# Kernel optimization log

Measured on AMD Instinct MI355X. Metric: run time of the kernel, lower is better.

Reference implementation:

```python
import jax, jax.numpy as jnp
import numpy as np

D_HEAD = 64
KV_HEADS = 8
Q_HEADS = 32
ROPE_BASE = 10000.0


def rope(x):
    # x: (B, S, H, D); pairs are interleaved along last dim, matching torch view(...,D//2,2)
    B, S, H, D = x.shape
    inv_freq = 1.0 / (ROPE_BASE ** (jnp.arange(0, D, 2, dtype=jnp.float32) / D))
    theta = jnp.arange(S, dtype=jnp.float32)[:, None] * inv_freq[None, :]  # (S, D/2)
    cos = jnp.cos(theta)[None, :, None, :]
    sin = jnp.sin(theta)[None, :, None, :]
    xf = x.astype(jnp.float32).reshape(B, S, H, D // 2, 2)
    x1, x2 = xf[..., 0], xf[..., 1]
    out = jnp.stack((x1 * cos - x2 * sin, x1 * sin + x2 * cos), axis=-1)
    return out.reshape(B, S, H, D).astype(x.dtype)


def setup_inputs() -> dict:
    key = jax.random.key(0)
    ks = jax.random.split(key, 5)
    B, S, D = 2, 2048, 2048
    scale = 1.0 / np.sqrt(D)
    return {
        "x": jax.random.normal(ks[0], (B, S, D), dtype=jnp.float32),
        "Wq": jax.random.normal(ks[1], (Q_HEADS * D_HEAD, D), dtype=jnp.float32) * scale,
        "Wk": jax.random.normal(ks[2], (KV_HEADS * D_HEAD, D), dtype=jnp.float32) * scale,
        "Wv": jax.random.normal(ks[3], (KV_HEADS * D_HEAD, D), dtype=jnp.float32) * scale,
        "Wo": jax.random.normal(ks[4], (D, D), dtype=jnp.float32) * scale,
    }


def reference(x, Wq, Wk, Wv, Wo):
    B, S, D = x.shape
    G = Q_HEADS // KV_HEADS  # query heads per kv head

    Q = (x @ Wq.T).reshape(B, S, Q_HEADS, D_HEAD)
    K = (x @ Wk.T).reshape(B, S, KV_HEADS, D_HEAD)
    V = (x @ Wv.T).reshape(B, S, KV_HEADS, D_HEAD)

    Q = rope(Q)
    K = rope(K)

    # (B, KV, G, S, Dh): group g of kv head h corresponds to q head h*G+g,
    # exactly matching repeat_interleave of K/V along head dim.
    Q = Q.transpose(0, 2, 1, 3).reshape(B, KV_HEADS, G, S, D_HEAD)
    K = K.transpose(0, 2, 1, 3)  # (B, KV, S, Dh)
    V = V.transpose(0, 2, 1, 3)

    scores = jnp.einsum("bkgsd,bktd->bkgst", Q, K) / np.sqrt(D_HEAD).astype(np.float32)
    causal_mask = jnp.tril(jnp.ones((S, S), dtype=bool))
    scores = jnp.where(causal_mask, scores, -jnp.inf)
    probs = jax.nn.softmax(scores, axis=-1)
    attn = jnp.einsum("bkgst,bktd->bkgsd", probs, V)

    attn = attn.reshape(B, Q_HEADS, S, D_HEAD).transpose(0, 2, 1, 3).reshape(B, S, D)
    return attn @ Wo.T
```

## Files before the change

### kernel.cpp

```cpp
#include <hip/hip_runtime.h>
#include <stdint.h>

#define S_LEN   2048
#define D_MODEL 2048
#define DKV     512

typedef __attribute__((ext_vector_type(8))) short short8;
typedef __attribute__((ext_vector_type(4))) float f32x4;
typedef __attribute__((ext_vector_type(4))) unsigned uint4v;

__device__ static inline unsigned short f2bf(float f) {
  unsigned u = __builtin_bit_cast(unsigned, f);
  u += 0x7FFFu + ((u >> 16) & 1u);
  return (unsigned short)(u >> 16);
}
__device__ static inline float bf2f(unsigned short h) {
  return __builtin_bit_cast(float, ((unsigned)h) << 16);
}
__device__ static inline unsigned packtrunc2(float f0, float f1) {
  return __builtin_amdgcn_perm(__builtin_bit_cast(unsigned, f1),
                               __builtin_bit_cast(unsigned, f0), 0x07060302u);
}

__device__ static inline void gload_lds16(const void* g, void* lds) {
  __builtin_amdgcn_global_load_lds((const __attribute__((address_space(1))) void*)g,
                                   (__attribute__((address_space(3))) void*)lds,
                                   16, 0, 0);
}

template <int N>
__device__ __forceinline__ void wait_vm() {
  if constexpr (N == 8)      asm volatile("s_waitcnt vmcnt(8)" ::: "memory");
  else if constexpr (N == 6) asm volatile("s_waitcnt vmcnt(6)" ::: "memory");
  else if constexpr (N == 4) asm volatile("s_waitcnt vmcnt(4)" ::: "memory");
  else if constexpr (N == 3) asm volatile("s_waitcnt vmcnt(3)" ::: "memory");
  else                       asm volatile("s_waitcnt vmcnt(0)" ::: "memory");
}

__device__ static inline void pl32swap(unsigned& a, unsigned& b) {
  asm volatile("v_permlane32_swap_b32 %0, %1" : "+v"(a), "+v"(b));
}
__device__ static inline void pl16swap(unsigned& a, unsigned& b) {
  asm volatile("v_permlane16_swap_b32 %0, %1" : "+v"(a), "+v"(b));
}

__global__ __launch_bounds__(256) void cvt_all_kernel(
    const float* __restrict__ x, const float* __restrict__ wq, const float* __restrict__ wk,
    const float* __restrict__ wv, const float* __restrict__ wo,
    unsigned short* __restrict__ xb, unsigned short* __restrict__ wqb,
    unsigned short* __restrict__ wkb, unsigned short* __restrict__ wvb,
    unsigned short* __restrict__ wob) {
  int i = blockIdx.x * 256 + threadIdx.x;
  const float* s; unsigned short* d;
  if (i < 1048576)      { s = x;  d = xb;  }
  else if (i < 1572864) { s = wq; d = wqb; i -= 1048576; }
  else if (i < 1703936) { s = wk; d = wkb; i -= 1572864; }
  else if (i < 1835008) { s = wv; d = wvb; i -= 1703936; }
  else                  { s = wo; d = wob; i -= 1835008; }
  const float4 a = ((const float4*)s)[i * 2];
  const float4 b = ((const float4*)s)[i * 2 + 1];
  unsigned short u[8] = {f2bf(a.x), f2bf(a.y), f2bf(a.z), f2bf(a.w),
                         f2bf(b.x), f2bf(b.y), f2bf(b.z), f2bf(b.w)};
  *(uint4*)(d + (size_t)i * 8) = *(const uint4*)u;
}

template <int BM, int CMODE, typename CT>
__device__ __forceinline__ void gemm_deep_body(
    const unsigned short* __restrict__ A, int lda,
    const unsigned short* __restrict__ B, int ldb,
    CT* __restrict__ C, int ldc, int m0, int n0, unsigned short* ldsu) {
  constexpr int MI = BM / 32;
  constexpr int NI = 4;
  constexpr int A_BYTES = BM * 64;
  constexpr int B_BYTES = 256 * 64;
  constexpr int TILE_BYTES = A_BYTES + B_BYTES;
  constexpr int AL = BM / 128;
  constexpr int LOADS = AL + 2;
  constexpr int VMS = 2 * LOADS;

  const int tid  = threadIdx.x;
  const int lane = tid & 63;
  const int w    = tid >> 6;
  const int wm   = w >> 2;
  const int wn   = w & 3;
  const int lcol = lane & 15;
  const int lq   = lane >> 4;
  char* const ldsb = (char*)ldsu;

  const int sl   = (lane & 7) ^ (lane >> 3);
  const int colg = (sl & 3) * 8;
  const unsigned short* gA[AL];
  const unsigned short* gB[2];
#pragma unroll
  for (int L = 0; L < AL; ++L) {
    const int r = 2 * (L * 64 + w * 8 + (lane >> 3)) + (sl >> 2);
    gA[L] = A + (size_t)(m0 + r) * lda + colg;
  }
#pragma unroll
  for (int L = 0; L < 2; ++L) {
    const int r = 2 * (L * 64 + w * 8 + (lane >> 3)) + (sl >> 2);
    gB[L] = B + (size_t)(n0 + r) * ldb + colg;
  }

  auto stage = [&](int tt) {
    char* const sb = ldsb + (tt & 3) * TILE_BYTES;
#pragma unroll
    for (int L = 0; L < AL; ++L)
      gload_lds16(gA[L] + tt * 32, sb + L * 8192 + w * 1024);
#pragma unroll
    for (int L = 0; L < 2; ++L)
      gload_lds16(gB[L] + tt * 32, sb + A_BYTES + L * 8192 + w * 1024);
  };

  const int sR    = (((lcol & 1) << 2) | lq) ^ ((lcol >> 1) & 7);
  const int rdoff = (lcol >> 1) * 128 + sR * 16;

  f32x4 acc[MI][NI] = {};

  auto compute_tile = [&](char* buf) {
    short8 af[MI], bfr[NI];
#pragma unroll
    for (int mi = 0; mi < MI; ++mi)
      af[mi] = *(const short8*)(buf + wm * (MI * 1024) + mi * 1024 + rdoff);
#pragma unroll
    for (int ni = 0; ni < NI; ++ni)
      bfr[ni] = *(const short8*)(buf + A_BYTES + wn * 4096 + ni * 1024 + rdoff);
    __builtin_amdgcn_s_setprio(1);
#pragma unroll
    for (int mi = 0; mi < MI; ++mi)
#pragma unroll
      for (int ni = 0; ni < NI; ++ni)
        acc[mi][ni] = __builtin_amdgcn_mfma_f32_16x16x32_bf16(af[mi], bfr[ni], acc[mi][ni], 0, 0, 0);
    __builtin_amdgcn_s_setprio(0);
  };

  stage(0); stage(1); stage(2);

#define GPHASE(T, VMW, DOSTG)                          \
  do {                                                 \
    wait_vm<VMW>();                                    \
    __builtin_amdgcn_s_barrier();                      \
    asm volatile("" ::: "memory");                     \
    __builtin_amdgcn_sched_barrier(0);                 \
    if (DOSTG) stage((T) + 3);                         \
    compute_tile(ldsb + ((T) & 3) * TILE_BYTES);       \
  } while (0)

  for (int t4 = 0; t4 < 15; ++t4) {
    const int t = t4 * 4;
    GPHASE(t + 0, VMS, true);
    GPHASE(t + 1, VMS, true);
    GPHASE(t + 2, VMS, true);
    GPHASE(t + 3, VMS, true);
  }
  GPHASE(60, VMS,   true);
  GPHASE(61, VMS,   false);
  GPHASE(62, LOADS, false);
  GPHASE(63, 0,     false);
#undef GPHASE

#pragma unroll
  for (int mi = 0; mi < MI; ++mi)
#pragma unroll
    for (int ni = 0; ni < NI; ++ni)
#pragma unroll
      for (int r = 0; r < 4; ++r) {
        const int row = m0 + wm * (MI * 16) + mi * 16 + lq * 4 + r;
        const int col = n0 + wn * 64 + ni * 16 + lcol;
        if constexpr (CMODE == 1) {
          C[((size_t)((row >> 11) * 512 + col)) * 2048 + (row & 2047)] = f2bf(acc[mi][ni][r]);
        } else if constexpr (CMODE == 2) {
          C[(size_t)row * ldc + col] = acc[mi][ni][r];
        } else {
          C[(size_t)row * ldc + col] = f2bf(acc[mi][ni][r]);
        }
      }
}

__global__ __launch_bounds__(512, 2) void qkv_gemm_kernel(
    const unsigned short* __restrict__ x,
    const unsigned short* __restrict__ Wq, const unsigned short* __restrict__ Wk,
    const unsigned short* __restrict__ Wv,
    unsigned short* __restrict__ Qo, unsigned short* __restrict__ Ko,
    unsigned short* __restrict__ Vt) {
  extern __shared__ __align__(16) unsigned short lds[];
  const int bid = blockIdx.x;
  const int swz = (bid & 7) * 24 + (bid >> 3);
  const int mt = swz / 12, nt = swz % 12;
  const int m0 = mt * 256;
  if (nt < 8)
    gemm_deep_body<256, 0, unsigned short>(x, D_MODEL, Wq, D_MODEL, Qo, D_MODEL, m0, nt * 256, lds);
  else if (nt < 10)
    gemm_deep_body<256, 0, unsigned short>(x, D_MODEL, Wk, D_MODEL, Ko, DKV, m0, (nt - 8) * 256, lds);
  else
    gemm_deep_body<256, 1, unsigned short>(x, D_MODEL, Wv, D_MODEL, Vt, DKV, m0, (nt - 10) * 256, lds);
}

__global__ __launch_bounds__(512, 2) void oproj_gemm_kernel(
    const unsigned short* __restrict__ A, const unsigned short* __restrict__ Wo,
    float* __restrict__ C) {
  extern __shared__ __align__(16) unsigned short lds[];
  const int bid = blockIdx.x;
  const int swz = (bid & 7) * 32 + (bid >> 3);
  const int mt = swz >> 3, nt = swz & 7;
  gemm_deep_body<128, 2, float>(A, D_MODEL, Wo, D_MODEL, C, D_MODEL, mt * 128, nt * 256, lds);
}

__global__ __launch_bounds__(256) void rope_both_kernel(unsigned short* __restrict__ Qb,
                                                        unsigned short* __restrict__ Kb) {
  int idx = blockIdx.x * 256 + threadIdx.x;
  unsigned short* X; int lgHalf; float scale;
  if (idx < 4194304) { X = Qb; lgHalf = 10; scale = 0.1803368801111244f; }
  else               { X = Kb; lgHalf = 8;  scale = 1.0f; idx -= 4194304; }
  const int half = 1 << lgHalf;
  const int r  = idx >> lgHalf;
  const int cp = idx & (half - 1);
  const int i  = cp & 31;
  const int s  = r & (S_LEN - 1);
  const float inv = exp2f(-13.287712379549449f * (float)(2 * i) * (1.0f / 64.0f));
  const float th  = (float)s * inv;
  const float c = cosf(th), sn = sinf(th);
  unsigned short* p = X + ((size_t)r << (lgHalf + 1)) + 2 * cp;
  const float x0 = bf2f(p[0]), x1 = bf2f(p[1]);
  p[0] = f2bf((x0 * c - x1 * sn) * scale);
  p[1] = f2bf((x0 * sn + x1 * c) * scale);
}

#define SOFTMAX_FRAG(Sv, lac, pf)                                              \
  do {                                                                         \
    float e0 = __builtin_amdgcn_exp2f(Sv[0][0]);                               \
    float e1 = __builtin_amdgcn_exp2f(Sv[0][1]);                               \
    float e2 = __builtin_amdgcn_exp2f(Sv[0][2]);                               \
    float e3 = __builtin_amdgcn_exp2f(Sv[0][3]);                               \
    unsigned dd0 = packtrunc2(e0, e1), dd1 = packtrunc2(e2, e3);               \
    lac += (e0 + e1) + (e2 + e3);                                              \
    e0 = __builtin_amdgcn_exp2f(Sv[1][0]);                                     \
    e1 = __builtin_amdgcn_exp2f(Sv[1][1]);                                     \
    e2 = __builtin_amdgcn_exp2f(Sv[1][2]);                                     \
    e3 = __builtin_amdgcn_exp2f(Sv[1][3]);                                     \
    unsigned dd2 = packtrunc2(e0, e1), dd3 = packtrunc2(e2, e3);               \
    lac += (e0 + e1) + (e2 + e3);                                              \
    e0 = __builtin_amdgcn_exp2f(Sv[2][0]);                                     \
    e1 = __builtin_amdgcn_exp2f(Sv[2][1]);                                     \
    e2 = __builtin_amdgcn_exp2f(Sv[2][2]);                                     \
    e3 = __builtin_amdgcn_exp2f(Sv[2][3]);                                     \
    unsigned dd4 = packtrunc2(e0, e1), dd5 = packtrunc2(e2, e3);               \
    lac += (e0 + e1) + (e2 + e3);                                              \
    e0 = __builtin_amdgcn_exp2f(Sv[3][0]);                                     \
    e1 = __builtin_amdgcn_exp2f(Sv[3][1]);                                     \
    e2 = __builtin_amdgcn_exp2f(Sv[3][2]);                                     \
    e3 = __builtin_amdgcn_exp2f(Sv[3][3]);                                     \
    unsigned dd6 = packtrunc2(e0, e1), dd7 = packtrunc2(e2, e3);               \
    lac += (e0 + e1) + (e2 + e3);                                              \
    pl32swap(dd0, dd2); pl32swap(dd1, dd3);                                    \
    pl32swap(dd4, dd6); pl32swap(dd5, dd7);                                    \
    pl16swap(dd0, dd2); pl16swap(dd1, dd3);                                    \
    pl16swap(dd4, dd6); pl16swap(dd5, dd7);                                    \
    const uint4v va_ = {dd0, dd1, dd2, dd3};                                   \
    const uint4v vb_ = {dd4, dd5, dd6, dd7};                                   \
    pf##0 = __builtin_bit_cast(short8, va_);                                   \
    pf##1 = __builtin_bit_cast(short8, vb_);                                   \
  } while (0)

__global__ __launch_bounds__(256, 2) void attn_kernel(const unsigned short* __restrict__ Q,
                                                      const unsigned short* __restrict__ K,
                                                      const unsigned short* __restrict__ Vt,
                                                      unsigned short* __restrict__ O) {
  const int hq = blockIdx.y;
  const int bb = blockIdx.z;
  const int hk = hq >> 2;
  const int tid  = threadIdx.x;
  const int lane = tid & 63;
  const int w    = tid >> 6;
  const int lcol = lane & 15;
  const int lq   = lane >> 4;
  const int trow = tid >> 2;
  const int tq   = (tid & 3) * 16;

  const int X   = blockIdx.x;
  const int qt0 = X, qt1 = 31 - X;

  __shared__ unsigned short Ks[2][64 * 72];
  __shared__ unsigned short Vts[2][64 * 72];

  const int prow = w * 16 + lcol;

  short8 qf00, qf01, qf10, qf11;
  {
    const unsigned short* g0 = Q + ((size_t)(bb * S_LEN + qt0 * 64 + prow)) * D_MODEL + hq * 64;
    const unsigned short* g1 = Q + ((size_t)(bb * S_LEN + qt1 * 64 + prow)) * D_MODEL + hq * 64;
    qf00 = *(const short8*)(g0 + lq * 8);
    qf01 = *(const short8*)(g0 + 32 + lq * 8);
    qf10 = *(const short8*)(g1 + lq * 8);
    qf11 = *(const short8*)(g1 + 32 + lq * 8);
  }

  uint4 kp0, kp1, vp0, vp1;
  {
    const unsigned short* gk = K + ((size_t)(bb * S_LEN + trow)) * DKV + hk * 64 + tq;
    kp0 = *(const uint4*)gk; kp1 = *(const uint4*)(gk + 8);
    const unsigned short* gv = Vt + ((size_t)(bb * DKV + hk * 64 + trow)) * S_LEN + tq;
    vp0 = *(const uint4*)gv; vp1 = *(const uint4*)(gv + 8);
  }

  f32x4 Oacc[2][4] = {};
  float lacc0 = 0.f, lacc1 = 0.f;

  const int tmax = qt1;
  for (int t = 0; t <= tmax; ++t) {
    const int bs = t & 1;
    *(uint4*)&Ks[bs][trow * 72 + tq]      = kp0;
    *(uint4*)&Ks[bs][trow * 72 + tq + 8]  = kp1;
    *(uint4*)&Vts[bs][trow * 72 + tq]     = vp0;
    *(uint4*)&Vts[bs][trow * 72 + tq + 8] = vp1;
    if (t < tmax) {
      const int t1 = (t + 1) * 64;
      const unsigned short* gk = K + ((size_t)(bb * S_LEN + t1 + trow)) * DKV + hk * 64 + tq;
      kp0 = *(const uint4*)gk; kp1 = *(const uint4*)(gk + 8);
      const unsigned short* gv = Vt + ((size_t)(bb * DKV + hk * 64 + trow)) * S_LEN + t1 + tq;
      vp0 = *(const uint4*)gv; vp1 = *(const uint4*)(gv + 8);
    }
    asm volatile("s_waitcnt lgkmcnt(0)" ::: "memory");
    __builtin_amdgcn_s_barrier();
    __builtin_amdgcn_sched_barrier(0);

    const bool a0 = (t <= qt0);

    f32x4 S0[4] = {}, S1[4] = {};
#pragma unroll
    for (int ks = 0; ks < 2; ++ks)
#pragma unroll
      for (int nt = 0; nt < 4; ++nt) {
        const short8 kf = *(const short8*)&Ks[bs][(nt * 16 + lcol) * 72 + ks * 32 + lq * 8];
        const short8 q0 = ks ? qf01 : qf00;
        const short8 q1 = ks ? qf11 : qf10;
        if (a0) S0[nt] = __builtin_amdgcn_mfma_f32_16x16x32_bf16(kf, q0, S0[nt], 0, 0, 0);
        S1[nt] = __builtin_amdgcn_mfma_f32_16x16x32_bf16(kf, q1, S1[nt], 0, 0, 0);
      }

    if (t == qt0) {
#pragma unroll
      for (int nt = 0; nt < 4; ++nt)
#pragma unroll
        for (int r = 0; r < 4; ++r)
          if (nt * 16 + lq * 4 + r > prow) S0[nt][r] = -1e30f;
    }
    if (t == qt1) {
#pragma unroll
      for (int nt = 0; nt < 4; ++nt)
#pragma unroll
        for (int r = 0; r < 4; ++r)
          if (nt * 16 + lq * 4 + r > prow) S1[nt][r] = -1e30f;
    }

    short8 pf00, pf01, pf10, pf11;
    if (a0) SOFTMAX_FRAG(S0, lacc0, pf0);
    SOFTMAX_FRAG(S1, lacc1, pf1);

#pragma unroll
    for (int ks = 0; ks < 2; ++ks)
#pragma unroll
      for (int dt = 0; dt < 4; ++dt) {
        const short8 vf = *(const short8*)&Vts[bs][(dt * 16 + lcol) * 72 + ks * 32 + lq * 8];
        const short8 p0 = ks ? pf01 : pf00;
        const short8 p1 = ks ? pf11 : pf10;
        if (a0) Oacc[0][dt] = __builtin_amdgcn_mfma_f32_16x16x32_bf16(vf, p0, Oacc[0][dt], 0, 0, 0);
        Oacc[1][dt] = __builtin_amdgcn_mfma_f32_16x16x32_bf16(vf, p1, Oacc[1][dt], 0, 0, 0);
      }
  }

  const int qts[2] = {qt0, qt1};
  const float laccs[2] = {lacc0, lacc1};
#pragma unroll
  for (int j = 0; j < 2; ++j) {
    float l = laccs[j];
    l += __shfl_xor(l, 16);
    l += __shfl_xor(l, 32);
    const float inv = 1.0f / l;
    const int qrow = qts[j] * 64 + prow;
#pragma unroll
    for (int dt = 0; dt < 4; ++dt) {
      unsigned short u[4] = {f2bf(Oacc[j][dt][0] * inv), f2bf(Oacc[j][dt][1] * inv),
                             f2bf(Oacc[j][dt][2] * inv), f2bf(Oacc[j][dt][3] * inv)};
      *(uint2*)&O[(size_t)(bb * S_LEN + qrow) * D_MODEL + hq * 64 + dt * 16 + lq * 4] =
          *(const uint2*)u;
    }
  }
}

extern "C" void kernel_launch(void* const* d_in, const int* in_sizes, int n_in,
                              void* d_out, int out_size, void* d_ws, size_t ws_size,
                              hipStream_t stream) {
  const float* x  = (const float*)d_in[0];
  const float* Wq = (const float*)d_in[1];
  const float* Wk = (const float*)d_in[2];
  const float* Wv = (const float*)d_in[3];
  const float* Wo = (const float*)d_in[4];
  float* out = (float*)d_out;

  unsigned short* Qb  = (unsigned short*)d_ws;
  unsigned short* Kb  = Qb  + (size_t)4096 * 2048;
  unsigned short* Vtg = Kb  + (size_t)4096 * 512;
  unsigned short* Ab  = Vtg + (size_t)1024 * 2048;
  unsigned short* xb  = Ab  + (size_t)4096 * 2048;
  unsigned short* Wqb = xb  + (size_t)4096 * 2048;
  unsigned short* Wkb = Wqb + (size_t)2048 * 2048;
  unsigned short* Wvb = Wkb + (size_t)512 * 2048;
  unsigned short* Wob = Wvb + (size_t)512 * 2048;

  static bool attr_set = false;
  if (!attr_set) {
    hipFuncSetAttribute(reinterpret_cast<const void*>(qkv_gemm_kernel),
                        hipFuncAttributeMaxDynamicSharedMemorySize, 131072);
    hipFuncSetAttribute(reinterpret_cast<const void*>(oproj_gemm_kernel),
                        hipFuncAttributeMaxDynamicSharedMemorySize, 98304);
    attr_set = true;
  }

  cvt_all_kernel<<<9216, 256, 0, stream>>>(x, Wq, Wk, Wv, Wo, xb, Wqb, Wkb, Wvb, Wob);

  qkv_gemm_kernel<<<192, 512, 131072, stream>>>(xb, Wqb, Wkb, Wvb, Qb, Kb, Vtg);
  rope_both_kernel<<<20480, 256, 0, stream>>>(Qb, Kb);
  attn_kernel<<<dim3(16, 32, 2), 256, 0, stream>>>(Qb, Kb, Vtg, Ab);
  oproj_gemm_kernel<<<256, 512, 98304, stream>>>(Ab, Wob, out);
}
```

Before: 285.4 us.

## Pipeline attention K/V loads via direct-to-LDS 4-stage swizzled buffers

The attention kernel's register-staged double buffer for K/V tiles is replaced by a 4-deep ring of LDS buffers filled with direct global-to-LDS loads, issued three tiles ahead and waited on with vmcnt counters. The LDS layout changes from padded rows to an XOR-swizzled 128-byte row layout so that fragment reads avoid bank conflicts. s_setprio is raised around the MFMA sections. The aim is to hide global load latency and cut the VGPR round-trip and LDS store instructions, at the cost of 64KB of LDS per block, which may limit the occupancy of two blocks per CU.

```diff
diff --git a/kernel.cpp b/kernel.cpp
--- a/kernel.cpp
+++ b/kernel.cpp
@@ -274,14 +274,11 @@
   const int w    = tid >> 6;
   const int lcol = lane & 15;
   const int lq   = lane >> 4;
-  const int trow = tid >> 2;
-  const int tq   = (tid & 3) * 16;
 
   const int X   = blockIdx.x;
   const int qt0 = X, qt1 = 31 - X;
 
-  __shared__ unsigned short Ks[2][64 * 72];
-  __shared__ unsigned short Vts[2][64 * 72];
+  __shared__ __align__(16) unsigned char KV[4][16384];
 
   const int prow = w * 16 + lcol;
 
@@ -295,79 +292,81 @@
     qf11 = *(const short8*)(g1 + 32 + lq * 8);
   }
 
-  uint4 kp0, kp1, vp0, vp1;
-  {
-    const unsigned short* gk = K + ((size_t)(bb * S_LEN + trow)) * DKV + hk * 64 + tq;
-    kp0 = *(const uint4*)gk; kp1 = *(const uint4*)(gk + 8);
-    const unsigned short* gv = Vt + ((size_t)(bb * DKV + hk * 64 + trow)) * S_LEN + tq;
-    vp0 = *(const uint4*)gv; vp1 = *(const uint4*)(gv + 8);
-  }
+  const int sr  = lane >> 3;
+  const int sc8 = (lane & 7) ^ sr;
+  const unsigned short* gK0 = K  + ((size_t)(bb * S_LEN + w * 16 + sr))     * DKV   + hk * 64 + sc8 * 8;
+  const unsigned short* gK1 = K  + ((size_t)(bb * S_LEN + w * 16 + 8 + sr)) * DKV   + hk * 64 + sc8 * 8;
+  const unsigned short* gV0 = Vt + ((size_t)(bb * DKV + hk * 64 + w * 16 + sr))     * S_LEN + sc8 * 8;
+  const unsigned short* gV1 = Vt + ((size_t)(bb * DKV + hk * 64 + w * 16 + 8 + sr)) * S_LEN + sc8 * 8;
+
+  auto stage = [&](int tt) {
+    unsigned char* sb = &KV[tt & 3][0];
+    gload_lds16(gK0 + (size_t)tt * 64 * DKV, sb + w * 2048);
+    gload_lds16(gK1 + (size_t)tt * 64 * DKV, sb + w * 2048 + 1024);
+    gload_lds16(gV0 + (size_t)tt * 64,       sb + 8192 + w * 2048);
+    gload_lds16(gV1 + (size_t)tt * 64,       sb + 8192 + w * 2048 + 1024);
+  };
+
+  const int c0 = (lq ^ (lcol & 7)) << 4;
 
   f32x4 Oacc[2][4] = {};
   float lacc0 = 0.f, lacc1 = 0.f;
 
   const int tmax = qt1;
-  for (int t = 0; t <= tmax; ++t) {
-    const int bs = t & 1;
-    *(uint4*)&Ks[bs][trow * 72 + tq]      = kp0;
-    *(uint4*)&Ks[bs][trow * 72 + tq + 8]  = kp1;
-    *(uint4*)&Vts[bs][trow * 72 + tq]     = vp0;
-    *(uint4*)&Vts[bs][trow * 72 + tq + 8] = vp1;
-    if (t < tmax) {
-      const int t1 = (t + 1) * 64;
-      const unsigned short* gk = K + ((size_t)(bb * S_LEN + t1 + trow)) * DKV + hk * 64 + tq;
-      kp0 = *(const uint4*)gk; kp1 = *(const uint4*)(gk + 8);
-      const unsigned short* gv = Vt + ((size_t)(bb * DKV + hk * 64 + trow)) * S_LEN + t1 + tq;
-      vp0 = *(const uint4*)gv; vp1 = *(const uint4*)(gv + 8);
-    }
-    asm volatile("s_waitcnt lgkmcnt(0)" ::: "memory");
-    __builtin_amdgcn_s_barrier();
-    __builtin_amdgcn_sched_barrier(0);
-
-    const bool a0 = (t <= qt0);
-
-    f32x4 S0[4] = {}, S1[4] = {};
-#pragma unroll
-    for (int ks = 0; ks < 2; ++ks)
-#pragma unroll
-      for (int nt = 0; nt < 4; ++nt) {
-        const short8 kf = *(const short8*)&Ks[bs][(nt * 16 + lcol) * 72 + ks * 32 + lq * 8];
-        const short8 q0 = ks ? qf01 : qf00;
-        const short8 q1 = ks ? qf11 : qf10;
-        if (a0) S0[nt] = __builtin_amdgcn_mfma_f32_16x16x32_bf16(kf, q0, S0[nt], 0, 0, 0);
-        S1[nt] = __builtin_amdgcn_mfma_f32_16x16x32_bf16(kf, q1, S1[nt], 0, 0, 0);
-      }
-
-    if (t == qt0) {
-#pragma unroll
-      for (int nt = 0; nt < 4; ++nt)
-#pragma unroll
-        for (int r = 0; r < 4; ++r)
-          if (nt * 16 + lq * 4 + r > prow) S0[nt][r] = -1e30f;
-    }
-    if (t == qt1) {
-#pragma unroll
-      for (int nt = 0; nt < 4; ++nt)
-#pragma unroll
-        for (int r = 0; r < 4; ++r)
-          if (nt * 16 + lq * 4 + r > prow) S1[nt][r] = -1e30f;
-    }
-
-    short8 pf00, pf01, pf10, pf11;
-    if (a0) SOFTMAX_FRAG(S0, lacc0, pf0);
-    SOFTMAX_FRAG(S1, lacc1, pf1);
-
-#pragma unroll
-    for (int ks = 0; ks < 2; ++ks)
-#pragma unroll
-      for (int dt = 0; dt < 4; ++dt) {
-        const short8 vf = *(const short8*)&Vts[bs][(dt * 16 + lcol) * 72 + ks * 32 + lq * 8];
-        const short8 p0 = ks ? pf01 : pf00;
-        const short8 p1 = ks ? pf11 : pf10;
-        if (a0) Oacc[0][dt] = __builtin_amdgcn_mfma_f32_16x16x32_bf16(vf, p0, Oacc[0][dt], 0, 0, 0);
-        Oacc[1][dt] = __builtin_amdgcn_mfma_f32_16x16x32_bf16(vf, p1, Oacc[1][dt], 0, 0, 0);
-      }
-  }
+
+  stage(0); stage(1); stage(2);
+
+#define AITER(T, VMW)                                                            \
+  do {                                                                           \
+    const int t_ = (T);                                                          \
+    wait_vm<VMW>();                                                              \
+    __builtin_amdgcn_s_barrier();                                                \
+    __builtin_amdgcn_sched_barrier(0);                                           \
+    if (t_ + 3 <= tmax) stage(t_ + 3);                                           \
+    const unsigned char* Kb_ = &KV[t_ & 3][0];                                   \
+    const unsigned char* Vb_ = &KV[t_ & 3][8192];                                \
+    const bool a0_ = (t_ <= qt0);                                                \
+    f32x4 S0[4] = {}, S1[4] = {};                                                \
+    __builtin_amdgcn_s_setprio(1);                                               \
+    for (int ks = 0; ks < 2; ++ks)                                               \
+      for (int nt = 0; nt < 4; ++nt) {                                           \
+        const short8 kf = *(const short8*)(Kb_ + (nt * 16 + lcol) * 128 + (c0 ^ (ks << 6))); \
+        const short8 q0 = ks ? qf01 : qf00;                                      \
+        const short8 q1 = ks ? qf11 : qf10;                                      \
+        if (a0_) S0[nt] = __builtin_amdgcn_mfma_f32_16x16x32_bf16(kf, q0, S0[nt], 0, 0, 0); \
+        S1[nt] = __builtin_amdgcn_mfma_f32_16x16x32_bf16(kf, q1, S1[nt], 0, 0, 0);          \
+      }                                                                          \
+    __builtin_amdgcn_s_setprio(0);                                               \
+    if (t_ == qt0) {                                                             \
+      for (int nt = 0; nt < 4; ++nt)                                             \
+        for (int r = 0; r < 4; ++r)                                              \
+          if (nt * 16 + lq * 4 + r > prow) S0[nt][r] = -1e30f;                   \
+    }                                                                            \
+    if (t_ == qt1) {                                                             \
+      for (int nt = 0; nt < 4; ++nt)                                             \
+        for (int r = 0; r < 4; ++r)                                              \
+          if (nt * 16 + lq * 4 + r > prow) S1[nt][r] = -1e30f;                   \
+    }                                                                            \
+    short8 pf00, pf01, pf10, pf11;                                               \
+    if (a0_) SOFTMAX_FRAG(S0, lacc0, pf0);                                       \
+    SOFTMAX_FRAG(S1, lacc1, pf1);                                                \
+    __builtin_amdgcn_s_setprio(1);                                               \
+    for (int ks = 0; ks < 2; ++ks)                                               \
+      for (int dt = 0; dt < 4; ++dt) {                                           \
+        const short8 vf = *(const short8*)(Vb_ + (dt * 16 + lcol) * 128 + (c0 ^ (ks << 6))); \
+        const short8 p0 = ks ? pf01 : pf00;                                      \
+        const short8 p1 = ks ? pf11 : pf10;                                      \
+        if (a0_) Oacc[0][dt] = __builtin_amdgcn_mfma_f32_16x16x32_bf16(vf, p0, Oacc[0][dt], 0, 0, 0); \
+        Oacc[1][dt] = __builtin_amdgcn_mfma_f32_16x16x32_bf16(vf, p1, Oacc[1][dt], 0, 0, 0);          \
+      }                                                                          \
+    __builtin_amdgcn_s_setprio(0);                                               \
+  } while (0)
+
+  int t = 0;
+  for (; t <= tmax - 2; ++t) AITER(t, 8);
+  AITER(t, 4); ++t;
+  AITER(t, 0);
+#undef AITER
 
   const int qts[2] = {qt0, qt1};
   const float laccs[2] = {lacc0, lacc1};
@@ -419,8 +418,8 @@
 
   cvt_all_kernel<<<9216, 256, 0, stream>>>(x, Wq, Wk, Wv, Wo, xb, Wqb, Wkb, Wvb, Wob);
 
-  qkv_gemm_kernel<<<192, 512, 131072, stream>>>(xb, Wqb, Wkb, Wvb, Qb, Kb, Vtg);
+  qkv_gemm_kernel<<<dim3(192), 512, 131072, stream>>>(xb, Wqb, Wkb, Wvb, Qb, Kb, Vtg);
   rope_both_kernel<<<20480, 256, 0, stream>>>(Qb, Kb);
   attn_kernel<<<dim3(16, 32, 2), 256, 0, stream>>>(Qb, Kb, Vtg, Ab);
-  oproj_gemm_kernel<<<256, 512, 98304, stream>>>(Ab, Wob, out);
-}
+  oproj_gemm_kernel<<<dim3(256), 512, 98304, stream>>>(Ab, Wob, out);
+}
```

New measurement: 296.1 us. +3.8%, slower.
